# Optimization experiments

Measured on AMD Instinct MI355X. Metric: run time of the kernel, lower is better.

## Reference

```python
import jax, jax.numpy as jnp
import numpy as np

H = 8
DK = 32
D_MODEL = H * DK


def _leaky(x):
    # LeakyReLU(negative_slope=0.1)
    return jnp.where(x > 0, x, 0.1 * x)


def _edge_feat(p_edge, W1, b1, W2, b2):
    # p_edge: [b, d_edge, n, n] -> [b, h, d_k, n, n]
    e = jnp.transpose(p_edge, (0, 2, 3, 1))          # [b, n, n, d_edge]
    e = _leaky(e @ W1 + b1) @ W2 + b2                # [b, n, n, d_model]
    b, n = e.shape[0], e.shape[1]
    e = e.reshape(b, n, n, H, DK)
    return jnp.transpose(e, (0, 3, 4, 1, 2))          # [b, h, d_k, n, n]


def setup_inputs() -> dict:
    key = jax.random.key(0)
    ks = jax.random.split(key, 24)
    b, n, d_model, d_edge, d_hidden = 2, 512, 256, 40, 32
    s = 0.05
    return {
        "query": jax.random.normal(ks[0], (b, n, d_model), jnp.float32),
        "key_": jax.random.normal(ks[1], (b, n, d_model), jnp.float32),
        "value": jax.random.normal(ks[2], (b, n, d_model), jnp.float32),
        "edges_att": jax.random.normal(ks[3], (b, d_edge, n, n), jnp.float32),
        "mask": jax.random.randint(ks[4], (b, n), 0, 2, jnp.int32),
        "Wq": jax.random.normal(ks[5], (d_model, d_model), jnp.float32) * s,
        "bq": jax.random.normal(ks[6], (d_model,), jnp.float32) * s,
        "Wk": jax.random.normal(ks[7], (d_model, d_model), jnp.float32) * s,
        "bk": jax.random.normal(ks[8], (d_model,), jnp.float32) * s,
        "Wv": jax.random.normal(ks[9], (d_model, d_model), jnp.float32) * s,
        "bv": jax.random.normal(ks[10], (d_model,), jnp.float32) * s,
        "Wo": jax.random.normal(ks[11], (d_model, d_model), jnp.float32) * s,
        "bo": jax.random.normal(ks[12], (d_model,), jnp.float32) * s,
        "rkW1": jax.random.normal(ks[13], (d_edge, d_hidden), jnp.float32) * s,
        "rkb1": jax.random.normal(ks[14], (d_hidden,), jnp.float32) * s,
        "rkW2": jax.random.normal(ks[15], (d_hidden, d_model), jnp.float32) * s,
        "rkb2": jax.random.normal(ks[16], (d_model,), jnp.float32) * s,
        "rvW1": jax.random.normal(ks[17], (d_edge, d_hidden), jnp.float32) * s,
        "rvb1": jax.random.normal(ks[18], (d_hidden,), jnp.float32) * s,
        "rvW2": jax.random.normal(ks[19], (d_hidden, d_model), jnp.float32) * s,
        "rvb2": jax.random.normal(ks[20], (d_model,), jnp.float32) * s,
        "u": jax.random.normal(ks[21], (H, DK), jnp.float32) * s,
        "v": jax.random.normal(ks[22], (H, DK), jnp.float32) * s,
    }


def reference(query, key_, value, edges_att, mask,
              Wq, bq, Wk, bk, Wv, bv, Wo, bo,
              rkW1, rkb1, rkW2, rkb2, rvW1, rvb1, rvW2, rvb2, u, v):
    b, n, _ = query.shape

    def proj(x, W, bb):
        return jnp.transpose((x @ W + bb).reshape(b, n, H, DK), (0, 2, 1, 3))  # [b,h,n,d_k]

    q = proj(query, Wq, bq)
    k = proj(key_, Wk, bk)
    val = proj(value, Wv, bv)

    relK = _edge_feat(edges_att, rkW1, rkb1, rkW2, rkb2)  # [b,h,d_k,n,n]
    relV = _edge_feat(edges_att, rvW1, rvb1, rvW2, rvb2)  # [b,h,d_k,n,n]

    inv = 1.0 / jnp.sqrt(jnp.asarray(DK, q.dtype))
    s1 = jnp.einsum('bhid,bhjd->bhij', q, k) * inv
    s2 = jnp.einsum('bhid,bhdij->bhij', q + k, relK) * inv
    s3 = jnp.einsum('bhid,hd->bhi', k, u)[..., None]      # broadcast over j
    s4 = jnp.einsum('bhdij,hd->bhij', relK, v)
    scores = s1 + s2 + s3 + s4
    scores = jnp.where(mask[:, None, None, :] == 0, jnp.asarray(-1e12, scores.dtype), scores)
    p = jax.nn.softmax(scores, axis=-1)                    # [b,h,n,n]

    o = jnp.einsum('bhij,bhjd->bhid', p, val) + jnp.einsum('bhij,bhdij->bhid', p, relV)
    x = jnp.transpose(o, (0, 2, 1, 3)).reshape(b, n, D_MODEL)
    return x @ Wo + bo
```

## Files before the change

### kernel.cpp

```cpp
#include <hip/hip_runtime.h>
#include <hip/hip_bf16.h>

#define HH 8
#define DKK 32
#define DM 256
#define NN 512
#define DE 40
#define DHID 32
#define CH 128

typedef __attribute__((ext_vector_type(4))) short short4v;
typedef __attribute__((ext_vector_type(8))) short short8v;
typedef __attribute__((ext_vector_type(4))) float f32x4;

__device__ __forceinline__ unsigned short f2bf(float x) {
    union { __hip_bfloat16 h; unsigned short u; } c;
    c.h = __float2bfloat16(x);
    return c.u;
}
__device__ __forceinline__ float bf2f(unsigned short u) {
    return __uint_as_float(((unsigned int)u) << 16);
}
__device__ __forceinline__ float bf_lo(unsigned int u){ return __uint_as_float(u << 16); }
__device__ __forceinline__ float bf_hi(unsigned int u){ return __uint_as_float(u & 0xffff0000u); }
__device__ __forceinline__ unsigned int pack2bf(float a, float b) {
    return (unsigned int)f2bf(a) | ((unsigned int)f2bf(b) << 16);
}
__device__ __forceinline__ short8v ld8(const unsigned short* p) {
    short4v lo = *(const short4v*)p;
    short4v hi = *(const short4v*)(p + 4);
    short8v r;
    r[0]=lo[0]; r[1]=lo[1]; r[2]=lo[2]; r[3]=lo[3];
    r[4]=hi[0]; r[5]=hi[1]; r[6]=hi[2]; r[7]=hi[3];
    return r;
}

__global__ __launch_bounds__(256) void proj_kernel(
    const float* __restrict__ query, const float* __restrict__ key_,
    const float* __restrict__ value,
    const float* __restrict__ Wq, const float* __restrict__ bq,
    const float* __restrict__ Wk, const float* __restrict__ bk,
    const float* __restrict__ Wv, const float* __restrict__ bv,
    float* __restrict__ Q, float* __restrict__ K, float* __restrict__ V,
    unsigned short* __restrict__ VbfT, int grpPerMat)
{
    const int m  = blockIdx.x / grpPerMat;
    const int r0 = (blockIdx.x % grpPerMat) * 4;
    const float* x; const float* W; const float* bb; float* dst;
    if (m == 0)      { x = query; W = Wq; bb = bq; dst = Q; }
    else if (m == 1) { x = key_;  W = Wk; bb = bk; dst = K; }
    else             { x = value; W = Wv; bb = bv; dst = V; }
    const int c = threadIdx.x;
    const float b0 = bb[c];
    float a0 = b0, a1 = b0, a2 = b0, a3 = b0;
    for (int k = 0; k < DM; ++k) {
        const float w = W[k*DM + c];
        a0 = fmaf(x[(size_t)(r0+0)*DM + k], w, a0);
        a1 = fmaf(x[(size_t)(r0+1)*DM + k], w, a1);
        a2 = fmaf(x[(size_t)(r0+2)*DM + k], w, a2);
        a3 = fmaf(x[(size_t)(r0+3)*DM + k], w, a3);
    }
    dst[(size_t)(r0+0)*DM + c] = a0;
    dst[(size_t)(r0+1)*DM + c] = a1;
    dst[(size_t)(r0+2)*DM + c] = a2;
    dst[(size_t)(r0+3)*DM + c] = a3;
    if (m == 2) {
        const int b = r0 >> 9, n0 = r0 & 511;
        unsigned int* vt = (unsigned int*)(VbfT + ((size_t)(b*DM + c))*NN + n0);
        vt[0] = pack2bf(a0, a1);
        vt[1] = pack2bf(a2, a3);
    }
}

__global__ __launch_bounds__(256) void pre_kernel(
    const float* __restrict__ Q, const float* __restrict__ K,
    const float* __restrict__ vvec,
    const float* __restrict__ rkW2, const float* __restrict__ rkb2,
    const float* __restrict__ rkW1, const float* __restrict__ rvW1,
    const float* __restrict__ rkb1, const float* __restrict__ rvb1,
    unsigned short* __restrict__ s1, float* __restrict__ gkw,
    unsigned short* __restrict__ w1w, float* __restrict__ biasw)
{
    const int bid = blockIdx.x;
    const int tid = threadIdx.x;
    __shared__ __align__(16) float sh[2*64*33];

    if (bid < 1024) {
        float (*Qt)[33] = (float(*)[33])sh;
        float (*Kt)[33] = (float(*)[33])(sh + 64*33);
        const int bh = bid >> 6, b = bh >> 3, hh = bh & 7;
        const int bx = bid & 63;
        const int ti = (bx >> 3) * 64, tj = (bx & 7) * 64;
        const int c = tid & 31, r0 = tid >> 5;
#pragma unroll
        for (int s = 0; s < 8; ++s) {
            Qt[r0 + 8*s][c] = Q[(size_t)(b*NN + ti + r0 + 8*s)*DM + hh*DKK + c];
            Kt[r0 + 8*s][c] = K[(size_t)(b*NN + tj + r0 + 8*s)*DM + hh*DKK + c];
        }
        __syncthreads();
        const int tx = tid & 15, ty = tid >> 4;
        float acc[4][4] = {};
#pragma unroll
        for (int k = 0; k < DKK; ++k) {
            float qv[4], kv[4];
#pragma unroll
            for (int u = 0; u < 4; ++u) { qv[u] = Qt[ty*4+u][k]; kv[u] = Kt[tx*4+u][k]; }
#pragma unroll
            for (int ri = 0; ri < 4; ++ri)
#pragma unroll
                for (int cj = 0; cj < 4; ++cj)
                    acc[ri][cj] = fmaf(qv[ri], kv[cj], acc[ri][cj]);
        }
        const float inv = 0.17677669529663687f;
#pragma unroll
        for (int ri = 0; ri < 4; ++ri) {
            ushort4 o;
            o.x = f2bf(acc[ri][0]*inv); o.y = f2bf(acc[ri][1]*inv);
            o.z = f2bf(acc[ri][2]*inv); o.w = f2bf(acc[ri][3]*inv);
            *(ushort4*)(s1 + ((size_t)(b*HH + hh)*NN + ti + ty*4 + ri)*NN + tj + tx*4) = o;
        }
    } else if (bid < 2048) {
        const int bi = bid - 1024;
        const int h = tid >> 5, l32 = tid & 31;
        const float inv = 0.17677669529663687f;
        float* wf = sh;
        wf[tid] = inv*(Q[(size_t)bi*DM + tid] + K[(size_t)bi*DM + tid]) + vvec[tid];
        __syncthreads();
        float acc = 0.f;
#pragma unroll
        for (int d4 = 0; d4 < DKK/4; ++d4) {
            const float4 w4 = *(const float4*)(rkW2 + (size_t)l32*DM + h*DKK + d4*4);
            const float4 f4 = *(const float4*)(&wf[h*DKK + d4*4]);
            acc = fmaf(w4.x, f4.x, acc); acc = fmaf(w4.y, f4.y, acc);
            acc = fmaf(w4.z, f4.z, acc); acc = fmaf(w4.w, f4.w, acc);
        }
        gkw[(size_t)bi*264 + tid] = acc;
        if (tid < HH) {
            float a2 = 0.f;
#pragma unroll
            for (int d = 0; d < DKK; ++d)
                a2 = fmaf(rkb2[tid*DKK + d], wf[tid*DKK + d], a2);
            gkw[(size_t)bi*264 + 256 + tid] = a2;
        }
    } else {
        const int n = tid >> 2, qd = tid & 3;
#pragma unroll
        for (int kk = 0; kk < 17; ++kk) {
            const int k = qd*17 + kk;
            float v = 0.f;
            if (k < DE) v = (n < 32) ? rkW1[k*DHID + n] : rvW1[k*DHID + (n-32)];
            w1w[n*68 + k] = f2bf(v);
        }
        if (tid < 64) biasw[tid] = (tid < 32) ? rkb1[tid] : rvb1[tid-32];
    }
}

__global__ __launch_bounds__(256, 5) void chunk_kernel(
    const float* __restrict__ edges, const int* __restrict__ mask,
    const unsigned short* __restrict__ VbfT,
    const unsigned short* __restrict__ s1u,
    const unsigned short* __restrict__ w1w, const float* __restrict__ biasw,
    const float* __restrict__ gkw,
    float* __restrict__ ws_m, float* __restrict__ ws_z,
    float* __restrict__ ws_A, float* __restrict__ ws_O)
{
    const int bid = blockIdx.x;
    const int bi = bid >> 2, cq = bid & 3;
    const int b  = bi >> 9;
    const int i  = bi & 511;
    const int j0 = cq*CH;
    const int tid = threadIdx.x;
    const int h = tid >> 5, l32 = tid & 31;
    const int wid = tid >> 6, lane = tid & 63;
    const int g = lane >> 4, q16 = lane & 15;
    const int jj = tid & 127, half = tid >> 7;

    __shared__ __align__(16) unsigned char uni[17408];
    __shared__ __align__(16) unsigned short W1bf[64*68];
    __shared__ __align__(16) float sc[HH*132];
    __shared__ __align__(16) float gKs[HH*DKK];
    __shared__ float c0Ks[HH];
    __shared__ float bias_l[64];

    unsigned short* E   = (unsigned short*)uni;
    unsigned short* hvT = (unsigned short*)uni;
    unsigned short* hk  = (unsigned short*)(uni + 8448);
    unsigned short* pb  = (unsigned short*)(uni + 8448);
    float* paccA = (float*)uni;

    const size_t ebase = (size_t)b*DE*NN*NN + (size_t)i*NN;

    float ev[20];
    {
        const float* ep = edges + ebase + j0 + jj;
#pragma unroll
        for (int u = 0; u < 20; ++u) ev[u] = ep[(size_t)(half*20+u)*NN*NN];
    }

    {
        const unsigned int* src = (const unsigned int*)w1w;
        unsigned int* dst = (unsigned int*)W1bf;
#pragma unroll
        for (int u = tid; u < 2176; u += 256) dst[u] = src[u];
        const float* gsrc = gkw + (size_t)bi*264;
        gKs[tid] = gsrc[tid];
        if (tid < HH) c0Ks[tid] = gsrc[256 + tid];
        if (tid < 64) bias_l[tid] = biasw[tid];
    }
    __syncthreads();

    float biasv[4];
#pragma unroll
    for (int nt = 0; nt < 4; ++nt) biasv[nt] = bias_l[nt*16 + q16];

    const unsigned short* vtb = VbfT + (size_t)b*DM*NN;
    const unsigned short* s1b = s1u + (size_t)b*HH*NN*NN + (size_t)i*NN;

    {
        unsigned int* Ed = (unsigned int*)&E[jj*68 + half*20];
#pragma unroll
        for (int u = 0; u < 10; ++u) Ed[u] = pack2bf(ev[2*u], ev[2*u+1]);
        if (half) {
            unsigned int* Ez = (unsigned int*)&E[jj*68 + 40];
#pragma unroll
            for (int z = 0; z < 12; ++z) Ez[z] = 0u;
        }
    }
    __syncthreads();

    f32x4 acc[2][4];
#pragma unroll
    for (int jt = 0; jt < 2; ++jt) {
        const int jn = wid*32 + jt*16 + q16;
        short8v a0 = ld8(&E[jn*68 + g*8]);
        short8v a1 = ld8(&E[jn*68 + 32 + g*8]);
#pragma unroll
        for (int nt = 0; nt < 4; ++nt) {
            const unsigned short* wp = &W1bf[(q16 + nt*16)*68 + g*8];
            f32x4 c;
            c[0] = biasv[nt]; c[1] = biasv[nt]; c[2] = biasv[nt]; c[3] = biasv[nt];
            c = __builtin_amdgcn_mfma_f32_16x16x32_bf16(a0, ld8(wp), c, 0, 0, 0);
            c = __builtin_amdgcn_mfma_f32_16x16x32_bf16(a1, ld8(wp + 32), c, 0, 0, 0);
            acc[jt][nt] = c;
        }
    }
    __syncthreads();

#pragma unroll
    for (int jt = 0; jt < 2; ++jt) {
        const int jw = wid*32 + jt*16 + g*4;
#pragma unroll
        for (int nt = 0; nt < 4; ++nt) {
#pragma unroll
            for (int r = 0; r < 4; ++r) {
                float x = acc[jt][nt][r];
                x = x > 0.f ? x : 0.1f*x;
                const unsigned short us = f2bf(x);
                const int n = nt*16 + q16;
                if (n < 32) hk[(jw+r)*34 + n] = us;
                else        hvT[(n-32)*132 + (jw+r)] = us;
            }
        }
    }
    __syncthreads();

    {
        unsigned int hku[16];
#pragma unroll
        for (int d = 0; d < 16; ++d) hku[d] = *(const unsigned int*)&hk[jj*34 + 2*d];
        const int mk = mask[b*NN + j0 + jj];
        float racc[4];
#pragma unroll
        for (int u = 0; u < 4; ++u) racc[u] = c0Ks[half*4 + u];
#pragma unroll
        for (int d = 0; d < 16; ++d) {
            const float lo = bf_lo(hku[d]), hi = bf_hi(hku[d]);
#pragma unroll
            for (int u = 0; u < 4; ++u) {
                const int hh = half*4 + u;
                racc[u] = fmaf(gKs[hh*DKK + 2*d],     lo, racc[u]);
                racc[u] = fmaf(gKs[hh*DKK + 2*d + 1], hi, racc[u]);
            }
        }
#pragma unroll
        for (int u = 0; u < 4; ++u) {
            const int hh = half*4 + u;
            float r = racc[u] + bf2f(s1b[(size_t)hh*NN*NN + j0 + jj]);
            if (mk == 0) r = -1e12f;
            sc[hh*132 + jj] = r;
        }
    }
    __syncthreads();

    {
        float sv[4];
        float mc = -3e38f;
#pragma unroll
        for (int k = 0; k < 4; ++k) { sv[k] = sc[h*132 + l32 + 32*k]; mc = fmaxf(mc, sv[k]); }
#pragma unroll
        for (int off = 16; off; off >>= 1) mc = fmaxf(mc, __shfl_xor(mc, off, 32));
        float zc = 0.f;
#pragma unroll
        for (int k = 0; k < 4; ++k) {
            const float e = __expf(sv[k] - mc);
            pb[h*132 + l32 + 32*k] = f2bf(e);
            zc += e;
        }
#pragma unroll
        for (int off = 16; off; off >>= 1) zc += __shfl_xor(zc, off, 32);
        if (l32 == 0) {
            ws_m[(size_t)bid*8 + h] = mc;
            ws_z[(size_t)bid*8 + h] = zc;
        }
    }
    __syncthreads();

    f32x4 ca0 = {0.f,0.f,0.f,0.f}, ca1 = {0.f,0.f,0.f,0.f};
    {
        short8v pA = ld8(&pb[q16*132 + wid*32 + g*8]);
        short8v b0 = ld8(&hvT[q16*132 + wid*32 + g*8]);
        short8v b1 = ld8(&hvT[(16+q16)*132 + wid*32 + g*8]);
        ca0 = __builtin_amdgcn_mfma_f32_16x16x32_bf16(pA, b0, ca0, 0, 0, 0);
        ca1 = __builtin_amdgcn_mfma_f32_16x16x32_bf16(pA, b1, ca1, 0, 0, 0);
    }

    {
        f32x4 co[4] = {{0,0,0,0},{0,0,0,0},{0,0,0,0},{0,0,0,0}};
#pragma unroll
        for (int ks = 0; ks < 4; ++ks) {
            short8v pB = ld8(&pb[q16*132 + ks*32 + g*8]);
#pragma unroll
            for (int t = 0; t < 4; ++t) {
                const int c_row = (wid<<6) + (t<<4) + q16;
                short8v aV = ld8(&vtb[(size_t)c_row*NN + j0 + ks*32 + g*8]);
                co[t] = __builtin_amdgcn_mfma_f32_16x16x32_bf16(aV, pB, co[t], 0, 0, 0);
            }
        }
#pragma unroll
        for (int t = 0; t < 4; ++t) {
            const int hstar = wid*2 + (t >> 1);
            if (q16 == hstar) {
#pragma unroll
                for (int r = 0; r < 4; ++r)
                    ws_O[(size_t)bid*256 + (wid<<6) + (t<<4) + (g<<2) + r] = co[t][r];
            }
        }
    }
    __syncthreads();

    if (g < 2) {
#pragma unroll
        for (int r = 0; r < 4; ++r) {
            const int hrow = g*4 + r;
            paccA[wid*256 + hrow*32 + q16]      = ca0[r];
            paccA[wid*256 + hrow*32 + 16 + q16] = ca1[r];
        }
    }
    __syncthreads();
    ws_A[(size_t)bid*256 + tid] = paccA[tid] + paccA[256+tid] + paccA[512+tid] + paccA[768+tid];
}

__global__ __launch_bounds__(256) void combine_kernel(
    const float* __restrict__ rvW2, const float* __restrict__ rvb2,
    const float* __restrict__ Wo, const float* __restrict__ bo,
    const float* __restrict__ ws_m, const float* __restrict__ ws_z,
    const float* __restrict__ ws_A, const float* __restrict__ ws_O,
    float* __restrict__ out)
{
    const int bi0 = blockIdx.x * 2;
    const int tid = threadIdx.x;
    const int h = tid >> 5;
    __shared__ float A_l[2][DM], o_l[2][DM];
    __shared__ float wqs[2][4][HH], rzs[2][HH];

    if (tid < 16) {
        const int r = tid >> 3, hh = tid & 7;
        const int bi = bi0 + r;
        float mv[4], zv[4];
#pragma unroll
        for (int q = 0; q < 4; ++q) {
            mv[q] = ws_m[(size_t)(bi*4+q)*8 + hh];
            zv[q] = ws_z[(size_t)(bi*4+q)*8 + hh];
        }
        const float mm = fmaxf(fmaxf(mv[0], mv[1]), fmaxf(mv[2], mv[3]));
        float zt = 0.f;
#pragma unroll
        for (int q = 0; q < 4; ++q) {
            const float w = __expf(mv[q] - mm);
            wqs[r][q][hh] = w;
            zt = fmaf(zv[q], w, zt);
        }
        rzs[r][hh] = 1.f / zt;
    }
    __syncthreads();

    float o1v[2];
#pragma unroll
    for (int r = 0; r < 2; ++r) {
        const int bi = bi0 + r;
        const float rz = rzs[r][h];
        float A = 0.f, o1 = 0.f;
#pragma unroll
        for (int q = 0; q < 4; ++q) {
            const float w = wqs[r][q][h];
            A  = fmaf(w, ws_A[(size_t)(bi*4+q)*256 + tid], A);
            o1 = fmaf(w, ws_O[(size_t)(bi*4+q)*256 + tid], o1);
        }
        A_l[r][tid] = A * rz;
        o1v[r] = o1 * rz;
    }
    __syncthreads();

#pragma unroll
    for (int r = 0; r < 2; ++r) {
        float o2 = rvb2[tid];
#pragma unroll
        for (int t = 0; t < DHID; ++t)
            o2 = fmaf(A_l[r][h*DKK + t], rvW2[(size_t)t*DM + tid], o2);
        o_l[r][tid] = o1v[r] + o2;
    }
    __syncthreads();

    float acc0 = bo[tid], acc1 = acc0;
#pragma unroll 4
    for (int k = 0; k < DM; ++k) {
        const float w = Wo[(size_t)k*DM + tid];
        acc0 = fmaf(o_l[0][k], w, acc0);
        acc1 = fmaf(o_l[1][k], w, acc1);
    }
    out[(size_t)(bi0+0)*DM + tid] = acc0;
    out[(size_t)(bi0+1)*DM + tid] = acc1;
}

extern "C" void kernel_launch(void* const* d_in, const int* in_sizes, int n_in,
                              void* d_out, int out_size, void* d_ws, size_t ws_size,
                              hipStream_t stream) {
    const float* query = (const float*)d_in[0];
    const float* key_  = (const float*)d_in[1];
    const float* value = (const float*)d_in[2];
    const float* edges = (const float*)d_in[3];
    const int*   mask  = (const int*)d_in[4];
    const float* Wq = (const float*)d_in[5];
    const float* bq = (const float*)d_in[6];
    const float* Wk = (const float*)d_in[7];
    const float* bk = (const float*)d_in[8];
    const float* Wv = (const float*)d_in[9];
    const float* bv = (const float*)d_in[10];
    const float* Wo = (const float*)d_in[11];
    const float* bo = (const float*)d_in[12];
    const float* rkW1 = (const float*)d_in[13];
    const float* rkb1 = (const float*)d_in[14];
    const float* rkW2 = (const float*)d_in[15];
    const float* rkb2 = (const float*)d_in[16];
    const float* rvW1 = (const float*)d_in[17];
    const float* rvb1 = (const float*)d_in[18];
    const float* rvW2 = (const float*)d_in[19];
    const float* rvb2 = (const float*)d_in[20];
    const float* vvec = (const float*)d_in[22];

    const int rows = in_sizes[0] / DM;
    const int nchunk = rows * 4;

    float* Qw   = (float*)d_ws;
    float* Kw   = Qw + (size_t)rows*DM;
    float* Vw   = Kw + (size_t)rows*DM;
    float* gkw  = Vw + (size_t)rows*DM;
    float* biasw = gkw + (size_t)rows*264;
    float* ws_m = biasw + 64;
    float* ws_z = ws_m + (size_t)nchunk*8;
    float* ws_A = ws_z + (size_t)nchunk*8;
    float* ws_O = ws_A + (size_t)nchunk*256;
    unsigned short* s1u  = (unsigned short*)(ws_O + (size_t)nchunk*256);
    unsigned short* VbfT = s1u + (size_t)2*HH*NN*NN;
    unsigned short* w1w  = VbfT + (size_t)2*DM*NN;

    hipLaunchKernelGGL(proj_kernel, dim3(3*rows/4), dim3(256), 0, stream,
                       query, key_, value, Wq, bq, Wk, bk, Wv, bv,
                       Qw, Kw, Vw, VbfT, rows/4);
    hipLaunchKernelGGL(pre_kernel, dim3(2*rows + 1), dim3(256), 0, stream,
                       Qw, Kw, vvec, rkW2, rkb2, rkW1, rvW1, rkb1, rvb1,
                       s1u, gkw, w1w, biasw);
    hipLaunchKernelGGL(chunk_kernel, dim3(nchunk), dim3(256), 0, stream,
                       edges, mask, VbfT, s1u, w1w, biasw, gkw,
                       ws_m, ws_z, ws_A, ws_O);
    hipLaunchKernelGGL(combine_kernel, dim3(rows/2), dim3(256), 0, stream,
                       rvW2, rvb2, Wo, bo, ws_m, ws_z, ws_A, ws_O, (float*)d_out);
}
```

Measured before the change: 115.6 us.

## Replace bf16 MFMA P·V with fp32 FMA and defer partial reductions to combine

The P·V product in chunk_kernel now uses scalar fp32 FMAs that read V directly, in place of bf16 MFMAs on a transposed bf16 V copy. This removes the VbfT write from proj_kernel. Each 64-thread team writes its own partial sums for A and O to a 4x larger workspace, and combine_kernel adds them, which drops two LDS reductions and barriers from chunk_kernel. The s1 and mask loads are hoisted to the top so they overlap the edge loads. The tradeoffs are more global traffic for V and the partials, and FMA throughput in place of matrix cores.

```diff
diff --git a/kernel.cpp b/kernel.cpp
--- a/kernel.cpp
+++ b/kernel.cpp
@@ -42,7 +42,7 @@
     const float* __restrict__ Wk, const float* __restrict__ bk,
     const float* __restrict__ Wv, const float* __restrict__ bv,
     float* __restrict__ Q, float* __restrict__ K, float* __restrict__ V,
-    unsigned short* __restrict__ VbfT, int grpPerMat)
+    int grpPerMat)
 {
     const int m  = blockIdx.x / grpPerMat;
     const int r0 = (blockIdx.x % grpPerMat) * 4;
@@ -64,12 +64,6 @@
     dst[(size_t)(r0+1)*DM + c] = a1;
     dst[(size_t)(r0+2)*DM + c] = a2;
     dst[(size_t)(r0+3)*DM + c] = a3;
-    if (m == 2) {
-        const int b = r0 >> 9, n0 = r0 & 511;
-        unsigned int* vt = (unsigned int*)(VbfT + ((size_t)(b*DM + c))*NN + n0);
-        vt[0] = pack2bf(a0, a1);
-        vt[1] = pack2bf(a2, a3);
-    }
 }
 
 __global__ __launch_bounds__(256) void pre_kernel(
@@ -157,12 +151,12 @@
 
 __global__ __launch_bounds__(256, 5) void chunk_kernel(
     const float* __restrict__ edges, const int* __restrict__ mask,
-    const unsigned short* __restrict__ VbfT,
+    const float* __restrict__ V,
     const unsigned short* __restrict__ s1u,
     const unsigned short* __restrict__ w1w, const float* __restrict__ biasw,
     const float* __restrict__ gkw,
     float* __restrict__ ws_m, float* __restrict__ ws_z,
-    float* __restrict__ ws_A, float* __restrict__ ws_O)
+    float* __restrict__ ws_A4, float* __restrict__ ws_O4)
 {
     const int bid = blockIdx.x;
     const int bi = bid >> 2, cq = bid & 3;
@@ -173,6 +167,7 @@
     const int h = tid >> 5, l32 = tid & 31;
     const int wid = tid >> 6, lane = tid & 63;
     const int g = lane >> 4, q16 = lane & 15;
+    const int team = tid >> 6, qq = tid & 63, hq = qq >> 3;
     const int jj = tid & 127, half = tid >> 7;
 
     __shared__ __align__(16) unsigned char uni[17408];
@@ -186,7 +181,6 @@
     unsigned short* hvT = (unsigned short*)uni;
     unsigned short* hk  = (unsigned short*)(uni + 8448);
     unsigned short* pb  = (unsigned short*)(uni + 8448);
-    float* paccA = (float*)uni;
 
     const size_t ebase = (size_t)b*DE*NN*NN + (size_t)i*NN;
 
@@ -196,6 +190,13 @@
 #pragma unroll
         for (int u = 0; u < 20; ++u) ev[u] = ep[(size_t)(half*20+u)*NN*NN];
     }
+    unsigned short s1v[4];
+    {
+        const unsigned short* s1b = s1u + (size_t)b*HH*NN*NN + (size_t)i*NN + j0 + jj;
+#pragma unroll
+        for (int u = 0; u < 4; ++u) s1v[u] = s1b[(size_t)(half*4+u)*NN*NN];
+    }
+    const int mk = mask[b*NN + j0 + jj];
 
     {
         const unsigned int* src = (const unsigned int*)w1w;
@@ -206,17 +207,7 @@
         gKs[tid] = gsrc[tid];
         if (tid < HH) c0Ks[tid] = gsrc[256 + tid];
         if (tid < 64) bias_l[tid] = biasw[tid];
-    }
-    __syncthreads();
-
-    float biasv[4];
-#pragma unroll
-    for (int nt = 0; nt < 4; ++nt) biasv[nt] = bias_l[nt*16 + q16];
-
-    const unsigned short* vtb = VbfT + (size_t)b*DM*NN;
-    const unsigned short* s1b = s1u + (size_t)b*HH*NN*NN + (size_t)i*NN;
-
-    {
+
         unsigned int* Ed = (unsigned int*)&E[jj*68 + half*20];
 #pragma unroll
         for (int u = 0; u < 10; ++u) Ed[u] = pack2bf(ev[2*u], ev[2*u+1]);
@@ -227,6 +218,10 @@
         }
     }
     __syncthreads();
+
+    float biasv[4];
+#pragma unroll
+    for (int nt = 0; nt < 4; ++nt) biasv[nt] = bias_l[nt*16 + q16];
 
     f32x4 acc[2][4];
 #pragma unroll
@@ -268,7 +263,6 @@
         unsigned int hku[16];
 #pragma unroll
         for (int d = 0; d < 16; ++d) hku[d] = *(const unsigned int*)&hk[jj*34 + 2*d];
-        const int mk = mask[b*NN + j0 + jj];
         float racc[4];
 #pragma unroll
         for (int u = 0; u < 4; ++u) racc[u] = c0Ks[half*4 + u];
@@ -285,7 +279,7 @@
 #pragma unroll
         for (int u = 0; u < 4; ++u) {
             const int hh = half*4 + u;
-            float r = racc[u] + bf2f(s1b[(size_t)hh*NN*NN + j0 + jj]);
+            float r = racc[u] + bf2f(s1v[u]);
             if (mk == 0) r = -1e12f;
             sc[hh*132 + jj] = r;
         }
@@ -323,48 +317,36 @@
         ca0 = __builtin_amdgcn_mfma_f32_16x16x32_bf16(pA, b0, ca0, 0, 0, 0);
         ca1 = __builtin_amdgcn_mfma_f32_16x16x32_bf16(pA, b1, ca1, 0, 0, 0);
     }
-
-    {
-        f32x4 co[4] = {{0,0,0,0},{0,0,0,0},{0,0,0,0},{0,0,0,0}};
-#pragma unroll
-        for (int ks = 0; ks < 4; ++ks) {
-            short8v pB = ld8(&pb[q16*132 + ks*32 + g*8]);
-#pragma unroll
-            for (int t = 0; t < 4; ++t) {
-                const int c_row = (wid<<6) + (t<<4) + q16;
-                short8v aV = ld8(&vtb[(size_t)c_row*NN + j0 + ks*32 + g*8]);
-                co[t] = __builtin_amdgcn_mfma_f32_16x16x32_bf16(aV, pB, co[t], 0, 0, 0);
-            }
-        }
-#pragma unroll
-        for (int t = 0; t < 4; ++t) {
-            const int hstar = wid*2 + (t >> 1);
-            if (q16 == hstar) {
-#pragma unroll
-                for (int r = 0; r < 4; ++r)
-                    ws_O[(size_t)bid*256 + (wid<<6) + (t<<4) + (g<<2) + r] = co[t][r];
-            }
-        }
-    }
-    __syncthreads();
+    float aO0 = 0.f, aO1 = 0.f, aO2 = 0.f, aO3 = 0.f;
+    {
+        const float* vrow = V + (size_t)b*NN*DM + (size_t)(j0 + team)*DM + qq*4;
+        const unsigned short* ph = pb + hq*132 + team;
+#pragma unroll 4
+        for (int it = 0; it < 32; ++it) {
+            const float p = bf2f(ph[4*it]);
+            const float4 v4 = *(const float4*)(vrow + (size_t)it*4*DM);
+            aO0 = fmaf(p, v4.x, aO0); aO1 = fmaf(p, v4.y, aO1);
+            aO2 = fmaf(p, v4.z, aO2); aO3 = fmaf(p, v4.w, aO3);
+        }
+    }
 
     if (g < 2) {
+        float* pa = ws_A4 + ((size_t)bid*4 + wid)*256;
 #pragma unroll
         for (int r = 0; r < 4; ++r) {
             const int hrow = g*4 + r;
-            paccA[wid*256 + hrow*32 + q16]      = ca0[r];
-            paccA[wid*256 + hrow*32 + 16 + q16] = ca1[r];
-        }
-    }
-    __syncthreads();
-    ws_A[(size_t)bid*256 + tid] = paccA[tid] + paccA[256+tid] + paccA[512+tid] + paccA[768+tid];
+            pa[hrow*32 + q16]      = ca0[r];
+            pa[hrow*32 + 16 + q16] = ca1[r];
+        }
+    }
+    *(float4*)(ws_O4 + ((size_t)bid*4 + team)*256 + qq*4) = make_float4(aO0, aO1, aO2, aO3);
 }
 
 __global__ __launch_bounds__(256) void combine_kernel(
     const float* __restrict__ rvW2, const float* __restrict__ rvb2,
     const float* __restrict__ Wo, const float* __restrict__ bo,
     const float* __restrict__ ws_m, const float* __restrict__ ws_z,
-    const float* __restrict__ ws_A, const float* __restrict__ ws_O,
+    const float* __restrict__ ws_A4, const float* __restrict__ ws_O4,
     float* __restrict__ out)
 {
     const int bi0 = blockIdx.x * 2;
@@ -403,8 +385,10 @@
 #pragma unroll
         for (int q = 0; q < 4; ++q) {
             const float w = wqs[r][q][h];
-            A  = fmaf(w, ws_A[(size_t)(bi*4+q)*256 + tid], A);
-            o1 = fmaf(w, ws_O[(size_t)(bi*4+q)*256 + tid], o1);
+            const float* pa = ws_A4 + ((size_t)(bi*4+q))*1024 + tid;
+            const float* po = ws_O4 + ((size_t)(bi*4+q))*1024 + tid;
+            A  = fmaf(w, (pa[0]+pa[256]) + (pa[512]+pa[768]), A);
+            o1 = fmaf(w, (po[0]+po[256]) + (po[512]+po[768]), o1);
         }
         A_l[r][tid] = A * rz;
         o1v[r] = o1 * rz;
@@ -461,28 +445,27 @@
     const int rows = in_sizes[0] / DM;
     const int nchunk = rows * 4;
 
-    float* Qw   = (float*)d_ws;
-    float* Kw   = Qw + (size_t)rows*DM;
-    float* Vw   = Kw + (size_t)rows*DM;
-    float* gkw  = Vw + (size_t)rows*DM;
+    float* Qw    = (float*)d_ws;
+    float* Kw    = Qw + (size_t)rows*DM;
+    float* Vw    = Kw + (size_t)rows*DM;
+    float* gkw   = Vw + (size_t)rows*DM;
     float* biasw = gkw + (size_t)rows*264;
-    float* ws_m = biasw + 64;
-    float* ws_z = ws_m + (size_t)nchunk*8;
-    float* ws_A = ws_z + (size_t)nchunk*8;
-    float* ws_O = ws_A + (size_t)nchunk*256;
-    unsigned short* s1u  = (unsigned short*)(ws_O + (size_t)nchunk*256);
-    unsigned short* VbfT = s1u + (size_t)2*HH*NN*NN;
-    unsigned short* w1w  = VbfT + (size_t)2*DM*NN;
+    float* ws_m  = biasw + 64;
+    float* ws_z  = ws_m + (size_t)nchunk*8;
+    float* ws_A4 = ws_z + (size_t)nchunk*8;
+    float* ws_O4 = ws_A4 + (size_t)nchunk*1024;
+    unsigned short* s1u = (unsigned short*)(ws_O4 + (size_t)nchunk*1024);
+    unsigned short* w1w = s1u + (size_t)2*HH*NN*NN;
 
     hipLaunchKernelGGL(proj_kernel, dim3(3*rows/4), dim3(256), 0, stream,
                        query, key_, value, Wq, bq, Wk, bk, Wv, bv,
-                       Qw, Kw, Vw, VbfT, rows/4);
+                       Qw, Kw, Vw, rows/4);
     hipLaunchKernelGGL(pre_kernel, dim3(2*rows + 1), dim3(256), 0, stream,
                        Qw, Kw, vvec, rkW2, rkb2, rkW1, rvW1, rkb1, rvb1,
                        s1u, gkw, w1w, biasw);
     hipLaunchKernelGGL(chunk_kernel, dim3(nchunk), dim3(256), 0, stream,
-                       edges, mask, VbfT, s1u, w1w, biasw, gkw,
-                       ws_m, ws_z, ws_A, ws_O);
+                       edges, mask, Vw, s1u, w1w, biasw, gkw,
+                       ws_m, ws_z, ws_A4, ws_O4);
     hipLaunchKernelGGL(combine_kernel, dim3(rows/2), dim3(256), 0, stream,
-                       rvW2, rvb2, Wo, bo, ws_m, ws_z, ws_A, ws_O, (float*)d_out);
-}
+                       rvW2, rvb2, Wo, bo, ws_m, ws_z, ws_A4, ws_O4, (float*)d_out);
+}
```

Result: faster. 112.8 us (-2.4%).
